# Kernel optimization log

Hardware: AMD Instinct MI355X
Metric: run time of the kernel (lower is better)

## Reference

```python
import jax, jax.numpy as jnp
import numpy as np

D_MODEL = 512
N_HEADS = 8
N_LAYERS = 2
EPS = 1e-5  # torch LayerNorm default


def _ln(x, w, b):
    m = x.mean(-1, keepdims=True)
    v = ((x - m) ** 2).mean(-1, keepdims=True)
    return (x - m) / jnp.sqrt(v + EPS) * w + b


def _mha(q, k, v, in_w, in_b, out_w, out_b, n_heads, mask=None):
    # matches torch.nn.MultiheadAttention (batch_first, packed in_proj of shape (3D, D))
    D = q.shape[-1]
    hd = D // n_heads
    Q = q @ in_w[:D].T + in_b[:D]
    K = k @ in_w[D:2 * D].T + in_b[D:2 * D]
    V = v @ in_w[2 * D:].T + in_b[2 * D:]
    def heads(t):
        B, T, _ = t.shape
        return t.reshape(B, T, n_heads, hd).transpose(0, 2, 1, 3)
    Qh, Kh, Vh = heads(Q), heads(K), heads(V)
    s = jnp.einsum('bhqd,bhkd->bhqk', Qh, Kh) / np.sqrt(hd).astype(np.float32)
    if mask is not None:
        s = s + mask
    a = jax.nn.softmax(s, axis=-1)
    o = jnp.einsum('bhqk,bhkd->bhqd', a, Vh)
    o = o.transpose(0, 2, 1, 3).reshape(q.shape[0], q.shape[1], D)
    return o @ out_w.T + out_b


def _forward(x, ts, ode_w1, ode_b1, ode_w2, ode_b2,
             gru_wih, gru_whh, gru_bih, gru_bhh, te_a, te_b,
             t_in_w, t_in_b, t_out_w, t_out_b, t_ln1_w, t_ln1_b, t_ln2_w, t_ln2_b,
             t_ff1_w, t_ff1_b, t_ff2_w, t_ff2_b, t_lnf_w, t_lnf_b,
             ca_in_w, ca_in_b, ca_out_w, ca_out_b, ca_lin_w, ca_lin_b, ca_ln_w, ca_ln_b):
    B, T, D = x.shape
    # --- RK4 'jump-ODE' states. In the source, h is overwritten with x[:, i] at the
    # end of every step, so state_i depends only on (x[:,i-1], x[:,i], dt_i):
    # fully parallel over T (no scan needed). ODEFunc assumed: MLP tanh.
    ode = lambda y: jnp.tanh(y @ ode_w1.T + ode_b1) @ ode_w2.T + ode_b2
    dt = (ts[:, 1:] - ts[:, :-1])[..., None]            # (B,T-1,1)
    delta = (x[:, 1:] - x[:, :-1]) / dt                  # (B,T-1,D)
    f1 = ode(delta)
    f2 = ode(delta + 0.5 * dt * f1)
    f3 = ode(delta + 0.5 * dt * f2)
    f4 = ode(delta + dt * f3)
    states = x[:, :-1] + dt / 6.0 * (f1 + 2 * f2 + 2 * f3 + f4)
    H = jnp.concatenate([jnp.zeros((B, 1, D), x.dtype), states], axis=1)
    # --- GRUCell recurrence over T (true dependency -> lax.scan)
    Hd = gru_whh.shape[1]
    gx = H @ gru_wih.T + gru_bih                         # (B,T,3H) precomputed input proj
    def gru_step(h, xg):
        gh = h @ gru_whh.T + gru_bhh
        r = jax.nn.sigmoid(xg[:, :Hd] + gh[:, :Hd])
        zz = jax.nn.sigmoid(xg[:, Hd:2 * Hd] + gh[:, Hd:2 * Hd])
        n = jnp.tanh(xg[:, 2 * Hd:] + r * gh[:, 2 * Hd:])
        h = (1 - zz) * n + zz * h
        return h, h
    _, Hs = jax.lax.scan(gru_step, jnp.zeros((B, Hd), x.dtype), gx.transpose(1, 0, 2))
    H = Hs.transpose(1, 0, 2)                            # (B,T,H)
    # --- TimeHybridEncoding: even channels <- interleaved [sin,cos], odd <- ramp
    n_freq = (D // 2) // 2
    freqs = jnp.exp(-jnp.linspace(0.0, np.log(10000.0 / 4.0), n_freq)) * (2.0 * np.pi / 4.0)
    phase = ts[..., None] * freqs                        # (B,T,n_freq)
    sc = jnp.stack([jnp.sin(phase), jnp.cos(phase)], axis=-1).reshape(B, T, -1)
    ramp = ts[..., None] * te_a + te_b                   # (B,T,D//2)
    tm = jnp.zeros((B, T, D), x.dtype).at[..., 0::2].set(sc).at[..., 1::2].set(ramp)
    z = x + tm
    # --- pre-norm TransformerEncoder with causal mask (relu FFN, final LayerNorm)
    mask = jnp.where(jnp.triu(jnp.ones((T, T), bool), 1), jnp.float32(-1e9), jnp.float32(0.0)).astype(x.dtype)
    for l in range(N_LAYERS):
        y = _ln(z, t_ln1_w[l], t_ln1_b[l])
        z = z + _mha(y, y, y, t_in_w[l], t_in_b[l], t_out_w[l], t_out_b[l], N_HEADS, mask)
        y = _ln(z, t_ln2_w[l], t_ln2_b[l])
        z = z + jax.nn.relu(y @ t_ff1_w[l].T + t_ff1_b[l]) @ t_ff2_w[l].T + t_ff2_b[l]
    z = _ln(z, t_lnf_w, t_lnf_b)
    # --- cross attention: query = GRU states, kv = transformer output
    attn = _mha(H, z, z, ca_in_w, ca_in_b, ca_out_w, ca_out_b, N_HEADS, None)
    H = _ln(H + attn @ ca_lin_w.T + ca_lin_b, ca_ln_w, ca_ln_b)
    return H


def setup_inputs() -> dict:
    key = jax.random.key(0)
    B, T, D, L = 8, 1024, D_MODEL, N_LAYERS
    ks = iter(jax.random.split(key, 48))
    nrm = lambda *s: 0.02 * jax.random.normal(next(ks), s, jnp.float32)
    x = jax.random.normal(next(ks), (B, T, D), jnp.float32)
    # strictly increasing, roughly-normalized timestamps
    ts = jnp.cumsum(jax.random.uniform(next(ks), (B, T), jnp.float32, 0.01, 1.0), axis=1) / T
    return dict(
        x=x, ts=ts,
        ode_w1=nrm(D, D), ode_b1=jnp.zeros((D,), jnp.float32),
        ode_w2=nrm(D, D), ode_b2=jnp.zeros((D,), jnp.float32),
        gru_wih=nrm(3 * D, D), gru_whh=nrm(3 * D, D),
        gru_bih=jnp.zeros((3 * D,), jnp.float32), gru_bhh=jnp.zeros((3 * D,), jnp.float32),
        te_a=nrm(D // 2), te_b=nrm(D // 2),
        t_in_w=nrm(L, 3 * D, D), t_in_b=jnp.zeros((L, 3 * D), jnp.float32),
        t_out_w=nrm(L, D, D), t_out_b=jnp.zeros((L, D), jnp.float32),
        t_ln1_w=jnp.ones((L, D), jnp.float32), t_ln1_b=jnp.zeros((L, D), jnp.float32),
        t_ln2_w=jnp.ones((L, D), jnp.float32), t_ln2_b=jnp.zeros((L, D), jnp.float32),
        t_ff1_w=nrm(L, 4 * D, D), t_ff1_b=jnp.zeros((L, 4 * D), jnp.float32),
        t_ff2_w=nrm(L, D, 4 * D), t_ff2_b=jnp.zeros((L, D), jnp.float32),
        t_lnf_w=jnp.ones((D,), jnp.float32), t_lnf_b=jnp.zeros((D,), jnp.float32),
        ca_in_w=nrm(3 * D, D), ca_in_b=jnp.zeros((3 * D,), jnp.float32),
        ca_out_w=nrm(D, D), ca_out_b=jnp.zeros((D,), jnp.float32),
        ca_lin_w=nrm(D, D), ca_lin_b=jnp.zeros((D,), jnp.float32),
        ca_ln_w=jnp.ones((D,), jnp.float32), ca_ln_b=jnp.zeros((D,), jnp.float32))


def reference(x, ts, ode_w1, ode_b1, ode_w2, ode_b2,
              gru_wih, gru_whh, gru_bih, gru_bhh, te_a, te_b,
              t_in_w, t_in_b, t_out_w, t_out_b, t_ln1_w, t_ln1_b, t_ln2_w, t_ln2_b,
              t_ff1_w, t_ff1_b, t_ff2_w, t_ff2_b, t_lnf_w, t_lnf_b,
              ca_in_w, ca_in_b, ca_out_w, ca_out_b, ca_lin_w, ca_lin_b, ca_ln_w, ca_ln_b):
    return _forward(x, ts, ode_w1, ode_b1, ode_w2, ode_b2,
                    gru_wih, gru_whh, gru_bih, gru_bhh, te_a, te_b,
                    t_in_w, t_in_b, t_out_w, t_out_b, t_ln1_w, t_ln1_b, t_ln2_w, t_ln2_b,
                    t_ff1_w, t_ff1_b, t_ff2_w, t_ff2_b, t_lnf_w, t_lnf_b,
                    ca_in_w, ca_in_b, ca_out_w, ca_out_b, ca_lin_w, ca_lin_b, ca_ln_w, ca_ln_b)
```

## Files before the change

kernel.cpp:

```cpp
#include <hip/hip_runtime.h>
#include <math.h>

#define BB 8
#define TT 1024
#define DM 512
#define ROWS (BB*TT)
#define ROWS1 (BB*(TT-1))
#define GRU_J 8
#define GRU_BLK (BB*64)

typedef __attribute__((ext_vector_type(4))) float f32x4;
typedef __attribute__((ext_vector_type(8))) short bf16x8;
typedef __attribute__((ext_vector_type(4))) short bf16x4;

__device__ __forceinline__ float sigm_(float v){ return 1.f/(1.f+expf(-v)); }

__device__ __forceinline__ unsigned short f2bf(float f){
  unsigned u = __float_as_uint(f);
  return (unsigned short)((u + 0x7FFFu + ((u>>16)&1u)) >> 16);
}

__global__ __launch_bounds__(256) void castw_kernel(const float* __restrict__ w,
    unsigned short* __restrict__ o, int n4)
{
  int i = blockIdx.x*256 + threadIdx.x;
  if (i < n4) {
    float4 v = ((const float4*)w)[i];
    ushort4 u;
    u.x = f2bf(v.x); u.y = f2bf(v.y); u.z = f2bf(v.z); u.w = f2bf(v.w);
    ((ushort4*)o)[i] = u;
  }
}

__global__ __launch_bounds__(256) void delta_kernel(const float* __restrict__ x,
    const float* __restrict__ ts, float* __restrict__ delta,
    unsigned short* __restrict__ delta16)
{
  size_t i = (size_t)blockIdx.x*256 + threadIdx.x;
  int d = (int)(i & (DM-1));
  int r = (int)(i >> 9);
  int b = r / (TT-1), ii = r % (TT-1);
  float dt = ts[b*TT+ii+1] - ts[b*TT+ii];
  float x1 = x[((size_t)b*TT+ii+1)*DM + d];
  float x0 = x[((size_t)b*TT+ii)*DM + d];
  float v = (x1 - x0) / dt;
  delta[i] = v;
  delta16[i] = f2bf(v);
}

template<int INIT, int WRITE_Y>
__global__ __launch_bounds__(256) void rk_kernel(float* __restrict__ acc,
    unsigned short* y16, const float* __restrict__ delta,
    const float* __restrict__ f, const float* __restrict__ ts,
    float wa, float cy)
{
  size_t i = (size_t)blockIdx.x*256 + threadIdx.x;
  int r = (int)(i >> 9);
  int b = r / (TT-1), ii = r % (TT-1);
  float fv = f[i];
  float a = INIT ? 0.f : acc[i];
  acc[i] = a + wa*fv;
  if (WRITE_Y) {
    float dt = ts[b*TT+ii+1] - ts[b*TT+ii];
    y16[i] = f2bf(delta[i] + cy*dt*fv);
  }
}

__global__ __launch_bounds__(256) void states_kernel(const float* __restrict__ x,
    const float* __restrict__ ts, const float* __restrict__ acc,
    unsigned short* __restrict__ hin16)
{
  size_t i = (size_t)blockIdx.x*256 + threadIdx.x;
  int d = (int)(i & (DM-1));
  int r = (int)(i >> 9);
  int b = r >> 10, t = r & (TT-1);
  float v = 0.f;
  if (t > 0) {
    int ii = t-1;
    float dt = ts[b*TT+ii+1] - ts[b*TT+ii];
    v = x[((size_t)b*TT+ii)*DM + d] + dt*(1.f/6.f)*acc[((size_t)b*(TT-1)+ii)*DM + d];
  }
  hin16[i] = f2bf(v);
}

__global__ __launch_bounds__(256) void timeenc_kernel(const float* __restrict__ x,
    const float* __restrict__ ts, const float* __restrict__ te_a,
    const float* __restrict__ te_b, float* __restrict__ z)
{
  size_t i = (size_t)blockIdx.x*256 + threadIdx.x;
  int d = (int)(i & (DM-1));
  int r = (int)(i >> 9);
  float t = ts[r];
  float tm;
  if (d & 1) {
    int j = d >> 1;
    tm = t*te_a[j] + te_b[j];
  } else {
    int fi = d >> 2;
    float fr = expf(-(float)fi * 0.061606661f) * 1.5707964f;
    float ph = t * fr;
    tm = ((d & 3) == 0) ? sinf(ph) : cosf(ph);
  }
  z[i] = x[i] + tm;
}

template<int BF>
__global__ __launch_bounds__(256) void ln_kernel(const float* __restrict__ x,
    const float* __restrict__ w, const float* __restrict__ b,
    void* __restrict__ outp)
{
  int row = blockIdx.x;
  int tid = threadIdx.x;
  const float* xr = x + (size_t)row*DM;
  float2 v = *(const float2*)(xr + tid*2);
  float s = v.x+v.y, sq = v.x*v.x + v.y*v.y;
  #pragma unroll
  for (int off=1; off<64; off<<=1){ s += __shfl_xor(s,off); sq += __shfl_xor(sq,off); }
  __shared__ float rs[4], rq[4];
  int wid = tid>>6;
  if ((tid&63)==0){ rs[wid]=s; rq[wid]=sq; }
  __syncthreads();
  s = rs[0]+rs[1]+rs[2]+rs[3];
  sq = rq[0]+rq[1]+rq[2]+rq[3];
  float mean = s*(1.f/DM);
  float var = sq*(1.f/DM) - mean*mean;
  float inv = rsqrtf(var + 1e-5f);
  float2 wv = *(const float2*)(w + tid*2);
  float2 bv = *(const float2*)(b + tid*2);
  float ox = (v.x-mean)*inv*wv.x + bv.x;
  float oy = (v.y-mean)*inv*wv.y + bv.y;
  if (BF) {
    ushort2 u; u.x = f2bf(ox); u.y = f2bf(oy);
    *(ushort2*)((unsigned short*)outp + (size_t)row*DM + tid*2) = u;
  } else {
    float2 o; o.x = ox; o.y = oy;
    *(float2*)((float*)outp + (size_t)row*DM + tid*2) = o;
  }
}

template<int ACT>
__global__ __launch_bounds__(256) void bgemm_kernel(
    const unsigned short* __restrict__ A16, const unsigned short* __restrict__ Wb,
    const float* __restrict__ bias, const float* res,
    float* C, unsigned short* Cb, int M, int N, int K, int ldc)
{
  __shared__ __align__(16) unsigned short Al[2][128][40];
  __shared__ __align__(16) unsigned short Wl[2][128][40];
  const int bm = blockIdx.y*128, bn = blockIdx.x*128;
  const int tid = threadIdx.x;
  const int lane = tid & 63, wid = tid >> 6;
  const int wm = (wid&1)*64, wn = (wid>>1)*64;
  const int fl = lane & 15, fk = (lane>>4)*8;
  const int sar = tid>>2, sac = (tid&3)*8;
  f32x4 acc[4][4];
  #pragma unroll
  for (int i=0;i<4;i++)
    #pragma unroll
    for (int j=0;j<4;j++) acc[i][j] = (f32x4){0.f,0.f,0.f,0.f};

  uint4 areg[2], wreg[2];
  const int nk = K >> 5;

  auto load_t = [&](int kt){
    int k0 = kt*32;
    #pragma unroll
    for (int r=0;r<2;r++){
      int gr = bm + sar + r*64;
      areg[r] = (gr < M) ? *(const uint4*)(A16 + (size_t)gr*K + k0 + sac)
                         : make_uint4(0u,0u,0u,0u);
      wreg[r] = *(const uint4*)(Wb + (size_t)(bn + sar + r*64)*K + k0 + sac);
    }
  };
  auto store_t = [&](int buf){
    #pragma unroll
    for (int r=0;r<2;r++){
      *(uint4*)&Al[buf][sar + r*64][sac] = areg[r];
      *(uint4*)&Wl[buf][sar + r*64][sac] = wreg[r];
    }
  };

  load_t(0); store_t(0);
  int buf = 0;
  for (int kt = 0; kt < nk; ++kt) {
    __syncthreads();
    if (kt+1 < nk) load_t(kt+1);
    bf16x8 av[4], wv[4];
    #pragma unroll
    for (int i=0;i<4;i++) av[i] = *(const bf16x8*)&Al[buf][wm + i*16 + fl][fk];
    #pragma unroll
    for (int j=0;j<4;j++) wv[j] = *(const bf16x8*)&Wl[buf][wn + j*16 + fl][fk];
    #pragma unroll
    for (int i=0;i<4;i++)
      #pragma unroll
      for (int j=0;j<4;j++)
        acc[i][j] = __builtin_amdgcn_mfma_f32_16x16x32_bf16(av[i], wv[j], acc[i][j], 0, 0, 0);
    if (kt+1 < nk) store_t(buf^1);
    buf ^= 1;
  }

  #pragma unroll
  for (int j=0;j<4;j++){
    int gn = bn + wn + j*16 + fl;
    float bv = bias[gn];
    #pragma unroll
    for (int i=0;i<4;i++){
      #pragma unroll
      for (int r=0;r<4;r++){
        int gm = bm + wm + i*16 + (lane>>4)*4 + r;
        if (gm >= M) continue;
        float v = acc[i][j][r] + bv;
        if (ACT==1) v = fmaxf(v, 0.f);
        if (ACT==2) v = tanhf(v);
        if (res) v += res[(size_t)gm*ldc + gn];
        if (C)  C[(size_t)gm*ldc + gn] = v;
        if (Cb) Cb[(size_t)gm*ldc + gn] = f2bf(v);
      }
    }
  }
}

template<int CAUSAL>
__global__ __launch_bounds__(256) void mattn_kernel(
    const unsigned short* __restrict__ QKV, unsigned short* __restrict__ O)
{
  __shared__ __align__(16) unsigned short Kl[32][72];
  __shared__ __align__(16) unsigned short Vt[64][36];
  __shared__ __align__(16) unsigned short Pl[4][16][40];
  const int b = blockIdx.x >> 3, h = blockIdx.x & 7;
  const int q0 = blockIdx.y * 64;
  const int tid = threadIdx.x;
  const int lane = tid & 63, wid = tid >> 6;
  const int lq = lane & 15, g = lane >> 4;
  const size_t rowbase = (size_t)b*TT;

  bf16x8 qf0, qf1;
  {
    const unsigned short* qp = QKV + (rowbase + q0 + wid*16 + lq)*1536 + h*64 + g*8;
    qf0 = *(const bf16x8*)qp;
    qf1 = *(const bf16x8*)(qp + 32);
  }
  f32x4 o[4];
  #pragma unroll
  for (int dt=0; dt<4; dt++) o[dt] = (f32x4){0.f,0.f,0.f,0.f};
  float mr[4] = {-1e30f,-1e30f,-1e30f,-1e30f};
  float Lr[4] = {0.f,0.f,0.f,0.f};

  const int nkt = CAUSAL ? (q0/32 + 2) : (TT/32);
  const int qwmax = q0 + wid*16 + 15;
  const int sr = tid >> 3, scol = (tid & 7) * 8;

  for (int kt = 0; kt < nkt; ++kt) {
    const int k0 = kt*32;
    __syncthreads();
    *(uint4*)&Kl[sr][scol] = *(const uint4*)(QKV + (rowbase + k0 + sr)*1536 + 512 + h*64 + scol);
    {
      uint4 vv = *(const uint4*)(QKV + (rowbase + k0 + sr)*1536 + 1024 + h*64 + scol);
      const unsigned short* vs = (const unsigned short*)&vv;
      #pragma unroll
      for (int i=0;i<8;i++) Vt[scol+i][sr] = vs[i];
    }
    __syncthreads();
    if (CAUSAL && k0 > qwmax) continue;

    f32x4 st0 = (f32x4){0.f,0.f,0.f,0.f}, st1 = (f32x4){0.f,0.f,0.f,0.f};
    {
      bf16x8 kb;
      kb = *(const bf16x8*)&Kl[lq][g*8];
      st0 = __builtin_amdgcn_mfma_f32_16x16x32_bf16(qf0, kb, st0, 0,0,0);
      kb = *(const bf16x8*)&Kl[lq][g*8+32];
      st0 = __builtin_amdgcn_mfma_f32_16x16x32_bf16(qf1, kb, st0, 0,0,0);
      kb = *(const bf16x8*)&Kl[16+lq][g*8];
      st1 = __builtin_amdgcn_mfma_f32_16x16x32_bf16(qf0, kb, st1, 0,0,0);
      kb = *(const bf16x8*)&Kl[16+lq][g*8+32];
      st1 = __builtin_amdgcn_mfma_f32_16x16x32_bf16(qf1, kb, st1, 0,0,0);
    }
    float s0[4], s1[4];
    #pragma unroll
    for (int r=0;r<4;r++){ s0[r] = st0[r]*0.125f; s1[r] = st1[r]*0.125f; }
    if (CAUSAL) {
      int kg0 = k0 + lq, kg1 = k0 + 16 + lq;
      #pragma unroll
      for (int r=0;r<4;r++){
        int qg = q0 + wid*16 + 4*g + r;
        if (kg0 > qg) s0[r] = -1e30f;
        if (kg1 > qg) s1[r] = -1e30f;
      }
    }
    #pragma unroll
    for (int r=0;r<4;r++){
      float v = fmaxf(s0[r], s1[r]);
      v = fmaxf(v, __shfl_xor(v,1));
      v = fmaxf(v, __shfl_xor(v,2));
      v = fmaxf(v, __shfl_xor(v,4));
      v = fmaxf(v, __shfl_xor(v,8));
      float mn = fmaxf(mr[r], v);
      float scl = expf(mr[r] - mn);
      mr[r] = mn;
      float p0 = expf(s0[r] - mn);
      float p1 = expf(s1[r] - mn);
      float lt = p0 + p1;
      lt += __shfl_xor(lt,1); lt += __shfl_xor(lt,2);
      lt += __shfl_xor(lt,4); lt += __shfl_xor(lt,8);
      Lr[r] = Lr[r]*scl + lt;
      o[0][r] *= scl; o[1][r] *= scl; o[2][r] *= scl; o[3][r] *= scl;
      Pl[wid][4*g+r][lq]    = f2bf(p0);
      Pl[wid][4*g+r][16+lq] = f2bf(p1);
    }
    bf16x8 ap = *(const bf16x8*)&Pl[wid][lq][g*8];
    #pragma unroll
    for (int dt=0; dt<4; dt++){
      bf16x4 a4 = *(const bf16x4*)&Vt[lq+16*dt][g*8];
      bf16x4 b4 = *(const bf16x4*)&Vt[lq+16*dt][g*8+4];
      bf16x8 vb = __builtin_shufflevector(a4, b4, 0,1,2,3,4,5,6,7);
      o[dt] = __builtin_amdgcn_mfma_f32_16x16x32_bf16(ap, vb, o[dt], 0,0,0);
    }
  }

  #pragma unroll
  for (int r=0;r<4;r++){
    float inv = 1.f / Lr[r];
    int qg = q0 + wid*16 + 4*g + r;
    unsigned short* op = O + (rowbase + qg)*DM + h*64 + lq;
    op[0]  = f2bf(o[0][r]*inv);
    op[16] = f2bf(o[1][r]*inv);
    op[32] = f2bf(o[2][r]*inv);
    op[48] = f2bf(o[3][r]*inv);
  }
}

__global__ __launch_bounds__(256) void gru_scan_kernel(
    const float* __restrict__ gx,
    const float* __restrict__ whh,
    const float* __restrict__ bhh,
    float* __restrict__ Hs,
    unsigned short* __restrict__ Hsb,
    unsigned long long* hbuf)
{
  __shared__ float wlds[3][GRU_J][512];
  __shared__ float hsp[512];
  const int blk = blockIdx.x;
  const int b = blk & 7;
  const int g = blk >> 3;
  const int j0 = g * GRU_J;
  const int tid = threadIdx.x;

  for (int idx = tid; idx < 3*GRU_J*512/4; idx += 256) {
    int f = idx*4;
    int gate = f >> 12;
    int rem = f & 4095;
    int jj = rem >> 9, k = rem & 511;
    *(float4*)&wlds[gate][jj][k] = *(const float4*)&whh[(size_t)(gate*512 + j0 + jj)*512 + k];
  }
  const int row = tid >> 5;
  const int kl = tid & 31;
  const bool fin = (kl == 0);
  float bh0=0.f, bh1=0.f, bh2=0.f;
  if (fin) { bh0 = bhh[j0+row]; bh1 = bhh[512+j0+row]; bh2 = bhh[1024+j0+row]; }
  __syncthreads();

  for (int t = 0; t < TT; t++) {
    float g0=0.f, g1=0.f, g2=0.f;
    if (fin) {
      const float* gxr = gx + ((size_t)b*TT + t)*1536 + j0 + row;
      g0 = gxr[0]; g1 = gxr[512]; g2 = gxr[1024];
    }
    if (t == 0) {
      hsp[tid] = 0.f; hsp[tid+256] = 0.f;
    } else {
      const unsigned want = (unsigned)t;
      unsigned long long* src = hbuf + ((size_t)((t-1)&1)*BB + b)*512;
      unsigned long long u0, u1;
      for (;;) {
        u0 = __hip_atomic_load(src + tid,       __ATOMIC_RELAXED, __HIP_MEMORY_SCOPE_AGENT);
        u1 = __hip_atomic_load(src + tid + 256, __ATOMIC_RELAXED, __HIP_MEMORY_SCOPE_AGENT);
        if (((unsigned)(u0>>32) == want) & ((unsigned)(u1>>32) == want)) break;
        __builtin_amdgcn_s_sleep(1);
      }
      hsp[tid]     = __uint_as_float((unsigned)u0);
      hsp[tid+256] = __uint_as_float((unsigned)u1);
    }
    __syncthreads();

    float s0=0.f, s1=0.f, s2=0.f;
    #pragma unroll
    for (int j=0;j<4;j++){
      int k = kl*4 + j*128;
      float4 h4 = *(const float4*)&hsp[k];
      float4 a = *(const float4*)&wlds[0][row][k];
      float4 c = *(const float4*)&wlds[1][row][k];
      float4 d = *(const float4*)&wlds[2][row][k];
      s0 += a.x*h4.x + a.y*h4.y + a.z*h4.z + a.w*h4.w;
      s1 += c.x*h4.x + c.y*h4.y + c.z*h4.z + c.w*h4.w;
      s2 += d.x*h4.x + d.y*h4.y + d.z*h4.z + d.w*h4.w;
    }
    #pragma unroll
    for (int off=1; off<32; off<<=1) {
      s0 += __shfl_xor(s0, off);
      s1 += __shfl_xor(s1, off);
      s2 += __shfl_xor(s2, off);
    }
    if (fin) {
      float r  = sigm_(g0 + s0 + bh0);
      float z  = sigm_(g1 + s1 + bh1);
      float n  = tanhf(g2 + r*(s2 + bh2));
      float hold = hsp[j0 + row];
      float hnew = (1.f - z)*n + z*hold;
      size_t off = ((size_t)b*TT + t)*DM + j0 + row;
      Hs[off]  = hnew;
      Hsb[off] = f2bf(hnew);
      unsigned long long pk = ((unsigned long long)(unsigned)(t+1) << 32) | __float_as_uint(hnew);
      __hip_atomic_store(&hbuf[((size_t)(t&1)*BB + b)*512 + j0 + row], pk,
                         __ATOMIC_RELAXED, __HIP_MEMORY_SCOPE_AGENT);
    }
    __syncthreads();
  }
}

static void launch_bgemm(int act, const unsigned short* A16, const unsigned short* Wb,
                         const float* bias, const float* res, float* C, unsigned short* Cb,
                         int M, int N, int K, int ldc, hipStream_t stream)
{
  dim3 grid(N/128, (M+127)/128), blk(256);
  switch(act){
    case 1: bgemm_kernel<1><<<grid,blk,0,stream>>>(A16,Wb,bias,res,C,Cb,M,N,K,ldc); break;
    case 2: bgemm_kernel<2><<<grid,blk,0,stream>>>(A16,Wb,bias,res,C,Cb,M,N,K,ldc); break;
    default: bgemm_kernel<0><<<grid,blk,0,stream>>>(A16,Wb,bias,res,C,Cb,M,N,K,ldc); break;
  }
}

static unsigned short* cast_w(const float* w, unsigned short* dst, size_t n, hipStream_t s)
{
  castw_kernel<<<((int)(n/4)+255)/256, 256, 0, s>>>(w, dst, (int)(n/4));
  return dst + n;
}

extern "C" void kernel_launch(void* const* d_in, const int* in_sizes, int n_in,
                              void* d_out, int out_size, void* d_ws, size_t ws_size,
                              hipStream_t stream)
{
  (void)in_sizes; (void)n_in; (void)out_size; (void)ws_size;
  const float* x       = (const float*)d_in[0];
  const float* ts      = (const float*)d_in[1];
  const float* ode_w1  = (const float*)d_in[2];
  const float* ode_b1  = (const float*)d_in[3];
  const float* ode_w2  = (const float*)d_in[4];
  const float* ode_b2  = (const float*)d_in[5];
  const float* gru_wih = (const float*)d_in[6];
  const float* gru_whh = (const float*)d_in[7];
  const float* gru_bih = (const float*)d_in[8];
  const float* gru_bhh = (const float*)d_in[9];
  const float* te_a    = (const float*)d_in[10];
  const float* te_b    = (const float*)d_in[11];
  const float* t_in_w  = (const float*)d_in[12];
  const float* t_in_b  = (const float*)d_in[13];
  const float* t_out_w = (const float*)d_in[14];
  const float* t_out_b = (const float*)d_in[15];
  const float* t_ln1_w = (const float*)d_in[16];
  const float* t_ln1_b = (const float*)d_in[17];
  const float* t_ln2_w = (const float*)d_in[18];
  const float* t_ln2_b = (const float*)d_in[19];
  const float* t_ff1_w = (const float*)d_in[20];
  const float* t_ff1_b = (const float*)d_in[21];
  const float* t_ff2_w = (const float*)d_in[22];
  const float* t_ff2_b = (const float*)d_in[23];
  const float* t_lnf_w = (const float*)d_in[24];
  const float* t_lnf_b = (const float*)d_in[25];
  const float* ca_in_w = (const float*)d_in[26];
  const float* ca_in_b = (const float*)d_in[27];
  const float* ca_out_w= (const float*)d_in[28];
  const float* ca_out_b= (const float*)d_in[29];
  const float* ca_lin_w= (const float*)d_in[30];
  const float* ca_lin_b= (const float*)d_in[31];
  const float* ca_ln_w = (const float*)d_in[32];
  const float* ca_ln_b = (const float*)d_in[33];

  float* ws = (float*)d_ws;
  const size_t SZ = (size_t)ROWS * DM;
  float* deltab = ws + 0*SZ;
  float* accb   = ws + 1*SZ;
  float* fcur   = ws + 2*SZ;
  float* gx     = ws + 3*SZ;
  float* zbuf   = ws + 6*SZ;
  float* hsb    = ws + 7*SZ;
  unsigned long long* hbuf = (unsigned long long*)(ws + 8*SZ);
  unsigned short* u16 = (unsigned short*)(ws + 8*SZ + 16384);
  unsigned short* delta16 = u16 + 0*SZ;
  unsigned short* y16     = u16 + 1*SZ;
  unsigned short* t16     = u16 + 2*SZ;
  unsigned short* hs16    = u16 + 3*SZ;
  unsigned short* ff1b16  = u16 + 4*SZ;
  unsigned short* qkv16   = ff1b16;
  unsigned short* ao16    = delta16;
  unsigned short* hin16   = y16;
  unsigned short* cao16   = y16;
  unsigned short* ln16    = t16;
  unsigned short* wp = u16 + 8*SZ;
  unsigned short* wb_ode1 = wp;  wp = cast_w(ode_w1,  wp, 512*512, stream);
  unsigned short* wb_ode2 = wp;  wp = cast_w(ode_w2,  wp, 512*512, stream);
  unsigned short* wb_gwih = wp;  wp = cast_w(gru_wih, wp, 1536*512, stream);
  unsigned short* wb_tin  = wp;  wp = cast_w(t_in_w,  wp, (size_t)2*1536*512, stream);
  unsigned short* wb_tout = wp;  wp = cast_w(t_out_w, wp, (size_t)2*512*512, stream);
  unsigned short* wb_ff1  = wp;  wp = cast_w(t_ff1_w, wp, (size_t)2*2048*512, stream);
  unsigned short* wb_ff2  = wp;  wp = cast_w(t_ff2_w, wp, (size_t)2*512*2048, stream);
  unsigned short* wb_cain = wp;  wp = cast_w(ca_in_w, wp, 1536*512, stream);
  unsigned short* wb_caout= wp;  wp = cast_w(ca_out_w,wp, 512*512, stream);
  unsigned short* wb_calin= wp;  wp = cast_w(ca_lin_w,wp, 512*512, stream);

  delta_kernel<<<ROWS1*DM/256, 256, 0, stream>>>(x, ts, deltab, delta16);
  const unsigned short* yin16 = delta16;
  const float was[4] = {1.f, 2.f, 2.f, 1.f};
  const float cys[4] = {0.5f, 0.5f, 1.f, 0.f};
  for (int s4 = 0; s4 < 4; s4++) {
    launch_bgemm(2, yin16, wb_ode1, ode_b1, nullptr, nullptr, t16, ROWS1, 512, 512, 512, stream);
    launch_bgemm(0, t16,  wb_ode2, ode_b2, nullptr, fcur, nullptr, ROWS1, 512, 512, 512, stream);
    if (s4 == 0)
      rk_kernel<1,1><<<ROWS1*DM/256,256,0,stream>>>(accb, y16, deltab, fcur, ts, was[s4], cys[s4]);
    else if (s4 < 3)
      rk_kernel<0,1><<<ROWS1*DM/256,256,0,stream>>>(accb, y16, deltab, fcur, ts, was[s4], cys[s4]);
    else
      rk_kernel<0,0><<<ROWS1*DM/256,256,0,stream>>>(accb, nullptr, deltab, fcur, ts, was[s4], 0.f);
    yin16 = y16;
  }
  states_kernel<<<ROWS*DM/256,256,0,stream>>>(x, ts, accb, hin16);

  launch_bgemm(0, hin16, wb_gwih, gru_bih, nullptr, gx, nullptr, ROWS, 1536, 512, 1536, stream);
  gru_scan_kernel<<<GRU_BLK, 256, 0, stream>>>(gx, gru_whh, gru_bhh, hsb, hs16, hbuf);

  timeenc_kernel<<<ROWS*DM/256,256,0,stream>>>(x, ts, te_a, te_b, zbuf);

  for (int l = 0; l < 2; l++) {
    ln_kernel<1><<<ROWS,256,0,stream>>>(zbuf, t_ln1_w + l*512, t_ln1_b + l*512, ln16);
    launch_bgemm(0, ln16, wb_tin + (size_t)l*1536*512, t_in_b + l*1536, nullptr, nullptr, qkv16, ROWS, 1536, 512, 1536, stream);
    mattn_kernel<1><<<dim3(64, TT/64), 256, 0, stream>>>(qkv16, ao16);
    launch_bgemm(0, ao16, wb_tout + (size_t)l*512*512, t_out_b + l*512, zbuf, zbuf, nullptr, ROWS, 512, 512, 512, stream);
    ln_kernel<1><<<ROWS,256,0,stream>>>(zbuf, t_ln2_w + l*512, t_ln2_b + l*512, ln16);
    launch_bgemm(1, ln16, wb_ff1 + (size_t)l*2048*512, t_ff1_b + l*2048, nullptr, nullptr, ff1b16, ROWS, 2048, 512, 2048, stream);
    launch_bgemm(0, ff1b16, wb_ff2 + (size_t)l*512*2048, t_ff2_b + l*512, zbuf, zbuf, nullptr, ROWS, 512, 2048, 512, stream);
  }
  ln_kernel<1><<<ROWS,256,0,stream>>>(zbuf, t_lnf_w, t_lnf_b, ln16);

  launch_bgemm(0, hs16, wb_cain,           ca_in_b,       nullptr, nullptr, qkv16,       ROWS,  512, 512, 1536, stream);
  launch_bgemm(0, ln16, wb_cain + 512*512, ca_in_b + 512, nullptr, nullptr, qkv16 + 512, ROWS, 1024, 512, 1536, stream);
  mattn_kernel<0><<<dim3(64, TT/64), 256, 0, stream>>>(qkv16, ao16);
  launch_bgemm(0, ao16, wb_caout, ca_out_b, nullptr, nullptr, cao16, ROWS, 512, 512, 512, stream);
  launch_bgemm(0, cao16, wb_calin, ca_lin_b, hsb, fcur, nullptr, ROWS, 512, 512, 512, stream);
  ln_kernel<0><<<ROWS,256,0,stream>>>(fcur, ca_ln_w, ca_ln_b, (float*)d_out);
}
```

Measured before the change: 3.197 ms.

## Fuse RK4 updates into ODE GEMM epilogue, add 64-wide tiles, merge weight casts

The RK4 accumulate/stage-input kernels and the states kernel are folded into the second ODE GEMM's epilogue, using per-row dt and source-row tables written by the delta kernel. This removes several full-size elementwise passes and the fp32 f buffer round trip. The GEMM gets a TN=64 tile variant for N=512 problems, which doubles the block count to improve occupancy and load balance. The ten weight-cast launches are merged into one kernel. The epilogue does more scattered global reads, and a separate tiny kernel zeroes the t=0 rows.

```diff
diff --git a/kernel.cpp b/kernel.cpp
--- a/kernel.cpp
+++ b/kernel.cpp
@@ -13,6 +13,13 @@
 typedef __attribute__((ext_vector_type(8))) short bf16x8;
 typedef __attribute__((ext_vector_type(4))) short bf16x4;
 
+struct RkArgs {
+  const float* delta; float* acc; unsigned short* y16;
+  const float* dtrow; const int* srcrow;
+  const float* x; unsigned short* hin16;
+  float wa, cy;
+};
+
 __device__ __forceinline__ float sigm_(float v){ return 1.f/(1.f+expf(-v)); }
 
 __device__ __forceinline__ unsigned short f2bf(float f){
@@ -20,21 +27,34 @@
   return (unsigned short)((u + 0x7FFFu + ((u>>16)&1u)) >> 16);
 }
 
-__global__ __launch_bounds__(256) void castw_kernel(const float* __restrict__ w,
-    unsigned short* __restrict__ o, int n4)
+__global__ __launch_bounds__(256) void castall_kernel(
+    const float* w0, const float* w1, const float* w2, const float* w3,
+    const float* w4, const float* w5, const float* w6, const float* w7,
+    const float* w8, const float* w9, unsigned short* __restrict__ o)
 {
   int i = blockIdx.x*256 + threadIdx.x;
-  if (i < n4) {
-    float4 v = ((const float4*)w)[i];
-    ushort4 u;
-    u.x = f2bf(v.x); u.y = f2bf(v.y); u.z = f2bf(v.z); u.w = f2bf(v.w);
-    ((ushort4*)o)[i] = u;
-  }
+  if (i >= 2228224) return;
+  const float* src; int off;
+  if      (i <   65536){ src=w0; off=0; }
+  else if (i <  131072){ src=w1; off=65536; }
+  else if (i <  327680){ src=w2; off=131072; }
+  else if (i <  720896){ src=w3; off=327680; }
+  else if (i <  851968){ src=w4; off=720896; }
+  else if (i < 1376256){ src=w5; off=851968; }
+  else if (i < 1900544){ src=w6; off=1376256; }
+  else if (i < 2097152){ src=w7; off=1900544; }
+  else if (i < 2162688){ src=w8; off=2097152; }
+  else                 { src=w9; off=2162688; }
+  float4 v = ((const float4*)src)[i - off];
+  ushort4 u;
+  u.x = f2bf(v.x); u.y = f2bf(v.y); u.z = f2bf(v.z); u.w = f2bf(v.w);
+  ((ushort4*)o)[i] = u;
 }
 
 __global__ __launch_bounds__(256) void delta_kernel(const float* __restrict__ x,
     const float* __restrict__ ts, float* __restrict__ delta,
-    unsigned short* __restrict__ delta16)
+    unsigned short* __restrict__ delta16,
+    float* __restrict__ dtrow, int* __restrict__ srcrow)
 {
   size_t i = (size_t)blockIdx.x*256 + threadIdx.x;
   int d = (int)(i & (DM-1));
@@ -46,41 +66,15 @@
   float v = (x1 - x0) / dt;
   delta[i] = v;
   delta16[i] = f2bf(v);
-}
-
-template<int INIT, int WRITE_Y>
-__global__ __launch_bounds__(256) void rk_kernel(float* __restrict__ acc,
-    unsigned short* y16, const float* __restrict__ delta,
-    const float* __restrict__ f, const float* __restrict__ ts,
-    float wa, float cy)
-{
-  size_t i = (size_t)blockIdx.x*256 + threadIdx.x;
-  int r = (int)(i >> 9);
-  int b = r / (TT-1), ii = r % (TT-1);
-  float fv = f[i];
-  float a = INIT ? 0.f : acc[i];
-  acc[i] = a + wa*fv;
-  if (WRITE_Y) {
-    float dt = ts[b*TT+ii+1] - ts[b*TT+ii];
-    y16[i] = f2bf(delta[i] + cy*dt*fv);
-  }
-}
-
-__global__ __launch_bounds__(256) void states_kernel(const float* __restrict__ x,
-    const float* __restrict__ ts, const float* __restrict__ acc,
-    unsigned short* __restrict__ hin16)
-{
-  size_t i = (size_t)blockIdx.x*256 + threadIdx.x;
-  int d = (int)(i & (DM-1));
-  int r = (int)(i >> 9);
-  int b = r >> 10, t = r & (TT-1);
-  float v = 0.f;
-  if (t > 0) {
-    int ii = t-1;
-    float dt = ts[b*TT+ii+1] - ts[b*TT+ii];
-    v = x[((size_t)b*TT+ii)*DM + d] + dt*(1.f/6.f)*acc[((size_t)b*(TT-1)+ii)*DM + d];
-  }
-  hin16[i] = f2bf(v);
+  if (d == 0) { dtrow[r] = dt; srcrow[r] = b*TT + ii; }
+}
+
+__global__ __launch_bounds__(256) void zero8_kernel(unsigned short* __restrict__ hin16)
+{
+  int tid = threadIdx.x;
+  for (int b = 0; b < BB; b++)
+    for (int k = tid; k < DM; k += 256)
+      hin16[(size_t)b*TT*DM + k] = 0;
 }
 
 __global__ __launch_bounds__(256) void timeenc_kernel(const float* __restrict__ x,
@@ -138,27 +132,28 @@
   }
 }
 
-template<int ACT>
+template<int ACT, int TN, int RKM>
 __global__ __launch_bounds__(256) void bgemm_kernel(
     const unsigned short* __restrict__ A16, const unsigned short* __restrict__ Wb,
     const float* __restrict__ bias, const float* res,
-    float* C, unsigned short* Cb, int M, int N, int K, int ldc)
-{
+    float* C, unsigned short* Cb, int M, int N, int K, int ldc, RkArgs rk)
+{
+  const int NJ = TN/32;
   __shared__ __align__(16) unsigned short Al[2][128][40];
-  __shared__ __align__(16) unsigned short Wl[2][128][40];
-  const int bm = blockIdx.y*128, bn = blockIdx.x*128;
+  __shared__ __align__(16) unsigned short Wl[2][TN][40];
+  const int bm = blockIdx.y*128, bn = blockIdx.x*TN;
   const int tid = threadIdx.x;
   const int lane = tid & 63, wid = tid >> 6;
-  const int wm = (wid&1)*64, wn = (wid>>1)*64;
+  const int wm = (wid&1)*64, wn = (wid>>1)*(TN/2);
   const int fl = lane & 15, fk = (lane>>4)*8;
   const int sar = tid>>2, sac = (tid&3)*8;
-  f32x4 acc[4][4];
+  f32x4 acc[4][NJ];
   #pragma unroll
   for (int i=0;i<4;i++)
     #pragma unroll
-    for (int j=0;j<4;j++) acc[i][j] = (f32x4){0.f,0.f,0.f,0.f};
-
-  uint4 areg[2], wreg[2];
+    for (int j=0;j<NJ;j++) acc[i][j] = (f32x4){0.f,0.f,0.f,0.f};
+
+  uint4 areg[2], wreg[TN/64];
   const int nk = K >> 5;
 
   auto load_t = [&](int kt){
@@ -168,15 +163,16 @@
       int gr = bm + sar + r*64;
       areg[r] = (gr < M) ? *(const uint4*)(A16 + (size_t)gr*K + k0 + sac)
                          : make_uint4(0u,0u,0u,0u);
+    }
+    #pragma unroll
+    for (int r=0;r<TN/64;r++)
       wreg[r] = *(const uint4*)(Wb + (size_t)(bn + sar + r*64)*K + k0 + sac);
-    }
   };
   auto store_t = [&](int buf){
     #pragma unroll
-    for (int r=0;r<2;r++){
-      *(uint4*)&Al[buf][sar + r*64][sac] = areg[r];
-      *(uint4*)&Wl[buf][sar + r*64][sac] = wreg[r];
-    }
+    for (int r=0;r<2;r++) *(uint4*)&Al[buf][sar + r*64][sac] = areg[r];
+    #pragma unroll
+    for (int r=0;r<TN/64;r++) *(uint4*)&Wl[buf][sar + r*64][sac] = wreg[r];
   };
 
   load_t(0); store_t(0);
@@ -184,22 +180,22 @@
   for (int kt = 0; kt < nk; ++kt) {
     __syncthreads();
     if (kt+1 < nk) load_t(kt+1);
-    bf16x8 av[4], wv[4];
+    bf16x8 av[4], wv[NJ];
     #pragma unroll
     for (int i=0;i<4;i++) av[i] = *(const bf16x8*)&Al[buf][wm + i*16 + fl][fk];
     #pragma unroll
-    for (int j=0;j<4;j++) wv[j] = *(const bf16x8*)&Wl[buf][wn + j*16 + fl][fk];
+    for (int j=0;j<NJ;j++) wv[j] = *(const bf16x8*)&Wl[buf][wn + j*16 + fl][fk];
     #pragma unroll
     for (int i=0;i<4;i++)
       #pragma unroll
-      for (int j=0;j<4;j++)
+      for (int j=0;j<NJ;j++)
         acc[i][j] = __builtin_amdgcn_mfma_f32_16x16x32_bf16(av[i], wv[j], acc[i][j], 0, 0, 0);
     if (kt+1 < nk) store_t(buf^1);
     buf ^= 1;
   }
 
   #pragma unroll
-  for (int j=0;j<4;j++){
+  for (int j=0;j<NJ;j++){
     int gn = bn + wn + j*16 + fl;
     float bv = bias[gn];
     #pragma unroll
@@ -211,9 +207,26 @@
         float v = acc[i][j][r] + bv;
         if (ACT==1) v = fmaxf(v, 0.f);
         if (ACT==2) v = tanhf(v);
-        if (res) v += res[(size_t)gm*ldc + gn];
-        if (C)  C[(size_t)gm*ldc + gn] = v;
-        if (Cb) Cb[(size_t)gm*ldc + gn] = f2bf(v);
+        if (RKM == 0) {
+          if (res) v += res[(size_t)gm*ldc + gn];
+          if (C)  C[(size_t)gm*ldc + gn] = v;
+          if (Cb) Cb[(size_t)gm*ldc + gn] = f2bf(v);
+        } else {
+          size_t idx = (size_t)gm*512 + gn;
+          float dt = rk.dtrow[gm];
+          if (RKM == 1) {
+            rk.acc[idx] = v;
+            rk.y16[idx] = f2bf(rk.delta[idx] + rk.cy*dt*v);
+          } else if (RKM == 2) {
+            rk.acc[idx] += rk.wa*v;
+            rk.y16[idx] = f2bf(rk.delta[idx] + rk.cy*dt*v);
+          } else {
+            float a = rk.acc[idx] + v;
+            int srow = rk.srcrow[gm];
+            rk.hin16[((size_t)srow+1)*512 + gn] =
+                f2bf(rk.x[(size_t)srow*512 + gn] + dt*(1.f/6.f)*a);
+          }
+        }
       }
     }
   }
@@ -416,22 +429,26 @@
   }
 }
 
-static void launch_bgemm(int act, const unsigned short* A16, const unsigned short* Wb,
+static RkArgs g_norm = {};
+
+static void launch_bgemm(int act, int tn, const unsigned short* A16, const unsigned short* Wb,
                          const float* bias, const float* res, float* C, unsigned short* Cb,
                          int M, int N, int K, int ldc, hipStream_t stream)
 {
-  dim3 grid(N/128, (M+127)/128), blk(256);
-  switch(act){
-    case 1: bgemm_kernel<1><<<grid,blk,0,stream>>>(A16,Wb,bias,res,C,Cb,M,N,K,ldc); break;
-    case 2: bgemm_kernel<2><<<grid,blk,0,stream>>>(A16,Wb,bias,res,C,Cb,M,N,K,ldc); break;
-    default: bgemm_kernel<0><<<grid,blk,0,stream>>>(A16,Wb,bias,res,C,Cb,M,N,K,ldc); break;
-  }
-}
-
-static unsigned short* cast_w(const float* w, unsigned short* dst, size_t n, hipStream_t s)
-{
-  castw_kernel<<<((int)(n/4)+255)/256, 256, 0, s>>>(w, dst, (int)(n/4));
-  return dst + n;
+  dim3 blk(256);
+  if (tn == 128) {
+    dim3 grid(N/128, (M+127)/128);
+    switch(act){
+      case 1: bgemm_kernel<1,128,0><<<grid,blk,0,stream>>>(A16,Wb,bias,res,C,Cb,M,N,K,ldc,g_norm); break;
+      default: bgemm_kernel<0,128,0><<<grid,blk,0,stream>>>(A16,Wb,bias,res,C,Cb,M,N,K,ldc,g_norm); break;
+    }
+  } else {
+    dim3 grid(N/64, (M+127)/128);
+    switch(act){
+      case 2: bgemm_kernel<2,64,0><<<grid,blk,0,stream>>>(A16,Wb,bias,res,C,Cb,M,N,K,ldc,g_norm); break;
+      default: bgemm_kernel<0,64,0><<<grid,blk,0,stream>>>(A16,Wb,bias,res,C,Cb,M,N,K,ldc,g_norm); break;
+    }
+  }
 }
 
 extern "C" void kernel_launch(void* const* d_in, const int* in_sizes, int n_in,
@@ -483,7 +500,9 @@
   float* zbuf   = ws + 6*SZ;
   float* hsb    = ws + 7*SZ;
   unsigned long long* hbuf = (unsigned long long*)(ws + 8*SZ);
-  unsigned short* u16 = (unsigned short*)(ws + 8*SZ + 16384);
+  float* dtrow  = ws + 8*SZ + 16384;
+  int*   srcrow = (int*)(ws + 8*SZ + 16384 + 8192);
+  unsigned short* u16 = (unsigned short*)(ws + 8*SZ + 16384 + 16384);
   unsigned short* delta16 = u16 + 0*SZ;
   unsigned short* y16     = u16 + 1*SZ;
   unsigned short* t16     = u16 + 2*SZ;
@@ -494,55 +513,62 @@
   unsigned short* hin16   = y16;
   unsigned short* cao16   = y16;
   unsigned short* ln16    = t16;
-  unsigned short* wp = u16 + 8*SZ;
-  unsigned short* wb_ode1 = wp;  wp = cast_w(ode_w1,  wp, 512*512, stream);
-  unsigned short* wb_ode2 = wp;  wp = cast_w(ode_w2,  wp, 512*512, stream);
-  unsigned short* wb_gwih = wp;  wp = cast_w(gru_wih, wp, 1536*512, stream);
-  unsigned short* wb_tin  = wp;  wp = cast_w(t_in_w,  wp, (size_t)2*1536*512, stream);
-  unsigned short* wb_tout = wp;  wp = cast_w(t_out_w, wp, (size_t)2*512*512, stream);
-  unsigned short* wb_ff1  = wp;  wp = cast_w(t_ff1_w, wp, (size_t)2*2048*512, stream);
-  unsigned short* wb_ff2  = wp;  wp = cast_w(t_ff2_w, wp, (size_t)2*512*2048, stream);
-  unsigned short* wb_cain = wp;  wp = cast_w(ca_in_w, wp, 1536*512, stream);
-  unsigned short* wb_caout= wp;  wp = cast_w(ca_out_w,wp, 512*512, stream);
-  unsigned short* wb_calin= wp;  wp = cast_w(ca_lin_w,wp, 512*512, stream);
-
-  delta_kernel<<<ROWS1*DM/256, 256, 0, stream>>>(x, ts, deltab, delta16);
+  unsigned short* wb = u16 + 8*SZ;
+  unsigned short* wb_ode1 = wb + 0;
+  unsigned short* wb_ode2 = wb + 262144;
+  unsigned short* wb_gwih = wb + 524288;
+  unsigned short* wb_tin  = wb + 1310720;
+  unsigned short* wb_tout = wb + 2883584;
+  unsigned short* wb_ff1  = wb + 3407872;
+  unsigned short* wb_ff2  = wb + 5505024;
+  unsigned short* wb_cain = wb + 7602176;
+  unsigned short* wb_caout= wb + 8388608;
+  unsigned short* wb_calin= wb + 8650752;
+
+  castall_kernel<<<(2228224+255)/256, 256, 0, stream>>>(
+      ode_w1, ode_w2, gru_wih, t_in_w, t_out_w, t_ff1_w, t_ff2_w,
+      ca_in_w, ca_out_w, ca_lin_w, wb);
+
+  delta_kernel<<<ROWS1*DM/256, 256, 0, stream>>>(x, ts, deltab, delta16, dtrow, srcrow);
+  RkArgs rk; rk.delta = deltab; rk.acc = accb; rk.y16 = y16;
+  rk.dtrow = dtrow; rk.srcrow = srcrow; rk.x = x; rk.hin16 = hin16;
   const unsigned short* yin16 = delta16;
   const float was[4] = {1.f, 2.f, 2.f, 1.f};
   const float cys[4] = {0.5f, 0.5f, 1.f, 0.f};
   for (int s4 = 0; s4 < 4; s4++) {
-    launch_bgemm(2, yin16, wb_ode1, ode_b1, nullptr, nullptr, t16, ROWS1, 512, 512, 512, stream);
-    launch_bgemm(0, t16,  wb_ode2, ode_b2, nullptr, fcur, nullptr, ROWS1, 512, 512, 512, stream);
+    launch_bgemm(2, 64, yin16, wb_ode1, ode_b1, nullptr, nullptr, t16, ROWS1, 512, 512, 512, stream);
+    rk.wa = was[s4]; rk.cy = cys[s4];
+    dim3 grid(512/64, (ROWS1+127)/128), blk(256);
     if (s4 == 0)
-      rk_kernel<1,1><<<ROWS1*DM/256,256,0,stream>>>(accb, y16, deltab, fcur, ts, was[s4], cys[s4]);
+      bgemm_kernel<0,64,1><<<grid,blk,0,stream>>>(t16, wb_ode2, ode_b2, nullptr, nullptr, nullptr, ROWS1, 512, 512, 512, rk);
     else if (s4 < 3)
-      rk_kernel<0,1><<<ROWS1*DM/256,256,0,stream>>>(accb, y16, deltab, fcur, ts, was[s4], cys[s4]);
+      bgemm_kernel<0,64,2><<<grid,blk,0,stream>>>(t16, wb_ode2, ode_b2, nullptr, nullptr, nullptr, ROWS1, 512, 512, 512, rk);
     else
-      rk_kernel<0,0><<<ROWS1*DM/256,256,0,stream>>>(accb, nullptr, deltab, fcur, ts, was[s4], 0.f);
+      bgemm_kernel<0,64,3><<<grid,blk,0,stream>>>(t16, wb_ode2, ode_b2, nullptr, nullptr, nullptr, ROWS1, 512, 512, 512, rk);
     yin16 = y16;
   }
-  states_kernel<<<ROWS*DM/256,256,0,stream>>>(x, ts, accb, hin16);
-
-  launch_bgemm(0, hin16, wb_gwih, gru_bih, nullptr, gx, nullptr, ROWS, 1536, 512, 1536, stream);
+  zero8_kernel<<<1, 256, 0, stream>>>(hin16);
+
+  launch_bgemm(0, 128, hin16, wb_gwih, gru_bih, nullptr, gx, nullptr, ROWS, 1536, 512, 1536, stream);
   gru_scan_kernel<<<GRU_BLK, 256, 0, stream>>>(gx, gru_whh, gru_bhh, hsb, hs16, hbuf);
 
   timeenc_kernel<<<ROWS*DM/256,256,0,stream>>>(x, ts, te_a, te_b, zbuf);
 
   for (int l = 0; l < 2; l++) {
     ln_kernel<1><<<ROWS,256,0,stream>>>(zbuf, t_ln1_w + l*512, t_ln1_b + l*512, ln16);
-    launch_bgemm(0, ln16, wb_tin + (size_t)l*1536*512, t_in_b + l*1536, nullptr, nullptr, qkv16, ROWS, 1536, 512, 1536, stream);
+    launch_bgemm(0, 128, ln16, wb_tin + (size_t)l*1536*512, t_in_b + l*1536, nullptr, nullptr, qkv16, ROWS, 1536, 512, 1536, stream);
     mattn_kernel<1><<<dim3(64, TT/64), 256, 0, stream>>>(qkv16, ao16);
-    launch_bgemm(0, ao16, wb_tout + (size_t)l*512*512, t_out_b + l*512, zbuf, zbuf, nullptr, ROWS, 512, 512, 512, stream);
+    launch_bgemm(0, 64, ao16, wb_tout + (size_t)l*512*512, t_out_b + l*512, zbuf, zbuf, nullptr, ROWS, 512, 512, 512, stream);
     ln_kernel<1><<<ROWS,256,0,stream>>>(zbuf, t_ln2_w + l*512, t_ln2_b + l*512, ln16);
-    launch_bgemm(1, ln16, wb_ff1 + (size_t)l*2048*512, t_ff1_b + l*2048, nullptr, nullptr, ff1b16, ROWS, 2048, 512, 2048, stream);
-    launch_bgemm(0, ff1b16, wb_ff2 + (size_t)l*512*2048, t_ff2_b + l*512, zbuf, zbuf, nullptr, ROWS, 512, 2048, 512, stream);
+    launch_bgemm(1, 128, ln16, wb_ff1 + (size_t)l*2048*512, t_ff1_b + l*2048, nullptr, nullptr, ff1b16, ROWS, 2048, 512, 2048, stream);
+    launch_bgemm(0, 64, ff1b16, wb_ff2 + (size_t)l*512*2048, t_ff2_b + l*512, zbuf, zbuf, nullptr, ROWS, 512, 2048, 512, stream);
   }
   ln_kernel<1><<<ROWS,256,0,stream>>>(zbuf, t_lnf_w, t_lnf_b, ln16);
 
-  launch_bgemm(0, hs16, wb_cain,           ca_in_b,       nullptr, nullptr, qkv16,       ROWS,  512, 512, 1536, stream);
-  launch_bgemm(0, ln16, wb_cain + 512*512, ca_in_b + 512, nullptr, nullptr, qkv16 + 512, ROWS, 1024, 512, 1536, stream);
+  launch_bgemm(0, 64,  hs16, wb_cain,           ca_in_b,       nullptr, nullptr, qkv16,       ROWS,  512, 512, 1536, stream);
+  launch_bgemm(0, 128, ln16, wb_cain + 512*512, ca_in_b + 512, nullptr, nullptr, qkv16 + 512, ROWS, 1024, 512, 1536, stream);
   mattn_kernel<0><<<dim3(64, TT/64), 256, 0, stream>>>(qkv16, ao16);
-  launch_bgemm(0, ao16, wb_caout, ca_out_b, nullptr, nullptr, cao16, ROWS, 512, 512, 512, stream);
-  launch_bgemm(0, cao16, wb_calin, ca_lin_b, hsb, fcur, nullptr, ROWS, 512, 512, 512, stream);
+  launch_bgemm(0, 64, ao16, wb_caout, ca_out_b, nullptr, nullptr, cao16, ROWS, 512, 512, 512, stream);
+  launch_bgemm(0, 64, cao16, wb_calin, ca_lin_b, hsb, fcur, nullptr, ROWS, 512, 512, 512, stream);
   ln_kernel<0><<<ROWS,256,0,stream>>>(fcur, ca_ln_w, ca_ln_b, (float*)d_out);
 }
```

Result: faster. 2.941 ms (-8.0%).
